# Kernel tuning notes

Hardware: AMD Instinct MI355X
Metric: run time of the kernel (lower is better)

The kernel has to match this reference:

```python
import jax, jax.numpy as jnp
import numpy as np

N = 50000          # nodes (num_sensors)
E = 600000         # edges
IN_DIM = 75        # 3 * 25
DIMS = [(75, 128), (128, 128), (128, 32)]  # (in, out) per layer: in->hidden->hidden->bottleneck


def setup_inputs() -> dict:
    key = jax.random.key(0)
    ks = jax.random.split(key, 4 + 5 * len(DIMS))
    inp = {
        "x": jax.random.normal(ks[0], (N, IN_DIM), dtype=jnp.float32),
        "edge_index": jax.random.randint(ks[1], (2, E), 0, N, dtype=jnp.int64),
        "weight": jax.random.uniform(ks[2], (E,), dtype=jnp.float32),
        "sim": jax.random.normal(ks[3], (E, 2), dtype=jnp.float32),
    }
    i = 4
    for l, (cin, cout) in enumerate(DIMS):
        s = jnp.float32(1.0 / np.sqrt(cin))
        inp[f"wr{l}"] = jax.random.normal(ks[i + 0], (cin, cout), dtype=jnp.float32) * s  # real part of complex conv filter
        inp[f"wi{l}"] = jax.random.normal(ks[i + 1], (cin, cout), dtype=jnp.float32) * s  # imag part
        inp[f"cb{l}"] = jnp.zeros((cout,), dtype=jnp.float32)                              # conv bias
        inp[f"lw{l}"] = jax.random.normal(ks[i + 2], (cout, cin), dtype=jnp.float32) * s  # Linear weight (torch layout [out,in])
        inp[f"lb{l}"] = jnp.zeros((cout,), dtype=jnp.float32)                              # Linear bias
        i += 5
    return inp


def _layer(x, src, dst, cr, ci, wr, wi, cb, lw, lb):
    # ModeConvFast: gather source features, scale by complex edge coefficient
    # c = weight * (sim_r + i*sim_i), scatter-add to destination nodes,
    # project with complex filter W = wr + i*wi, keep real part, add bias.
    xs = x[src]                                   # [E, Cin] gather
    agg_r = jax.ops.segment_sum(xs * cr[:, None], dst, num_segments=N)  # [N, Cin]
    agg_i = jax.ops.segment_sum(xs * ci[:, None], dst, num_segments=N)  # [N, Cin]
    conv = agg_r @ wr - agg_i @ wi + cb           # real part of complex matmul
    return jax.nn.relu(conv + x @ lw.T + lb)      # conv(x,...) + lin(x), then relu


def reference(x, edge_index, weight, sim,
              wr0, wi0, cb0, lw0, lb0,
              wr1, wi1, cb1, lw1, lb1,
              wr2, wi2, cb2, lw2, lb2):
    src, dst = edge_index[0], edge_index[1]
    cr = weight * sim[:, 0]                       # [E] real edge coefficient
    ci = weight * sim[:, 1]                       # [E] imag edge coefficient
    layers = [
        (wr0, wi0, cb0, lw0, lb0),
        (wr1, wi1, cb1, lw1, lb1),
        (wr2, wi2, cb2, lw2, lb2),
    ]
    for p in layers:
        x = _layer(x, src, dst, cr, ci, *p)
    return x
```

## Files before the change

kernel.cpp:

```cpp
#include <hip/hip_runtime.h>

#define N_NODES 50000
#define N_EDGES 600000
#define E_PAD_MAX (N_EDGES + N_NODES * 7)

using bf16x8 = __attribute__((ext_vector_type(8))) short;
using f32x4  = __attribute__((ext_vector_type(4))) float;
typedef unsigned int uint32_tt;

__device__ __forceinline__ unsigned short f2bf(float f) {
    union { float f; unsigned int u; } v; v.f = f;
    unsigned int u = v.u;
    return (unsigned short)((u + 0x7fffu + ((u >> 16) & 1u)) >> 16);
}
__device__ __forceinline__ float bf2f(unsigned int h16) {
    union { unsigned int u; float f; } v; v.u = h16 << 16;
    return v.f;
}


__global__ void hist_kernel(const int* __restrict__ ei, int* __restrict__ cnt, int E) {
    int e = blockIdx.x * 256 + threadIdx.x;
    if (e < E) atomicAdd(&cnt[ei[E + e]], 1);
}

__global__ void scan1(const int* __restrict__ deg, int* __restrict__ out,
                      int* __restrict__ bsum, int n) {
    __shared__ int s[256];
    int t = threadIdx.x;
    int base = blockIdx.x * 1024 + t * 4;
    int v0 = (base + 0 < n) ? ((deg[base + 0] + 7) & ~7) : 0;
    int v1 = (base + 1 < n) ? ((deg[base + 1] + 7) & ~7) : 0;
    int v2 = (base + 2 < n) ? ((deg[base + 2] + 7) & ~7) : 0;
    int v3 = (base + 3 < n) ? ((deg[base + 3] + 7) & ~7) : 0;
    int tsum = v0 + v1 + v2 + v3;
    s[t] = tsum;
    __syncthreads();
    for (int off = 1; off < 256; off <<= 1) {
        int tmp = (t >= off) ? s[t - off] : 0;
        __syncthreads();
        s[t] += tmp;
        __syncthreads();
    }
    int excl = s[t] - tsum;
    if (base + 0 < n) out[base + 0] = excl;
    if (base + 1 < n) out[base + 1] = excl + v0;
    if (base + 2 < n) out[base + 2] = excl + v0 + v1;
    if (base + 3 < n) out[base + 3] = excl + v0 + v1 + v2;
    if (t == 255) bsum[blockIdx.x] = s[255];
}

__global__ void scan2(int* __restrict__ bsum, int nb) {
    if (threadIdx.x == 0 && blockIdx.x == 0) {
        int acc = 0;
        for (int i = 0; i < nb; ++i) { int v = bsum[i]; bsum[i] = acc; acc += v; }
        bsum[nb] = acc;
    }
}

__global__ void scan3(int* __restrict__ off, const int* __restrict__ bsum, int n, int nb) {
    int i = blockIdx.x * 256 + threadIdx.x;
    if (i < n) off[i] += bsum[i >> 10];
    if (i == n) off[n] = bsum[nb];
}

__global__ void scatter_kernel(const int* __restrict__ ei, const float* __restrict__ w,
                               const float* __restrict__ sim, const int* __restrict__ off,
                               int* __restrict__ cnt, uint2* __restrict__ edat, int E) {
    int e = blockIdx.x * 256 + threadIdx.x;
    if (e >= E) return;
    int s = ei[e], d = ei[E + e];
    int p = off[d] + atomicAdd(&cnt[d], 1);
    float wt = w[e];
    uint2 m;
    m.x = (unsigned)s;
    m.y = (uint32_tt)f2bf(wt * sim[2 * e]) |
          ((uint32_tt)f2bf(wt * sim[2 * e + 1]) << 16);
    edat[p] = m;
}


__global__ void convert_x(const float* __restrict__ x0, unsigned short* __restrict__ xb, int n) {
    int i = blockIdx.x * 256 + threadIdx.x;
    if (i >= n * 96) return;
    int r = i / 96, c = i - r * 96;
    xb[i] = (c < 75) ? f2bf(x0[r * 75 + c]) : (unsigned short)0;
}

__global__ void build_bt(const float* __restrict__ wr, const float* __restrict__ wi,
                         const float* __restrict__ lw, unsigned short* __restrict__ BT,
                         int CIN, int CINP, int COUT) {
    int KTOT = 3 * CINP;
    int i = blockIdx.x * 256 + threadIdx.x;
    if (i >= COUT * KTOT) return;
    int nn = i / KTOT, k = i - nn * KTOT;
    int part = k / CINP, kk = k - part * CINP;
    float v = 0.f;
    if (kk < CIN) {
        if (part == 0)      v = wr[kk * COUT + nn];
        else if (part == 1) v = -wi[kk * COUT + nn];
        else                v = lw[nn * CIN + kk];
    }
    BT[i] = f2bf(v);
}

__global__ void build_bty(const float* __restrict__ wr, const float* __restrict__ wi,
                          const float* __restrict__ lw, unsigned short* __restrict__ BT) {
    int i = blockIdx.x * 256 + threadIdx.x;
    if (i >= 96 * 128) return;
    int nn = i >> 7, k = i & 127;
    float v;
    if (nn < 32)      v = wr[k * 32 + nn];
    else if (nn < 64) v = -wi[k * 32 + (nn - 32)];
    else              v = lw[(nn - 64) * 128 + k];
    BT[i] = f2bf(v);
}

template <int CU2>
__global__ __launch_bounds__(256) void agg_bf16(
    const uint32_tt* __restrict__ x, const int* __restrict__ off,
    const uint2* __restrict__ edat, uint32_tt* __restrict__ aggR,
    uint32_tt* __restrict__ aggI, int n) {
    int wave = threadIdx.x >> 6;
    int lane = threadIdx.x & 63;
    int node = __builtin_amdgcn_readfirstlane(blockIdx.x * 4 + wave);
    if (node >= n) return;
    int lc = (CU2 == 64) ? lane : (lane < CU2 ? lane : CU2 - 1);
    float arl = 0.f, arh = 0.f, ail = 0.f, aih = 0.f;
    int e0 = __builtin_amdgcn_readfirstlane(off[node]);
    int e1 = __builtin_amdgcn_readfirstlane(off[node + 1]);

    if (e0 < e1) {
        uint2 m[8];
#pragma unroll
        for (int j = 0; j < 8; ++j) m[j] = edat[e0 + j];
        for (int e = e0; e < e1; e += 8) {
            int sj[8]; float crj[8], cij[8];
#pragma unroll
            for (int j = 0; j < 8; ++j) {
                sj[j] = __builtin_amdgcn_readfirstlane((int)m[j].x);
                int pk = __builtin_amdgcn_readfirstlane((int)m[j].y);
                crj[j] = bf2f((unsigned)pk & 0xffffu);
                cij[j] = bf2f((unsigned)pk >> 16);
            }
            uint32_tt w[8];
#pragma unroll
            for (int j = 0; j < 8; ++j) {
                const uint32_tt* rowp = x + (size_t)sj[j] * CU2;
                w[j] = rowp[lc];
            }
            if (e + 8 < e1) {
#pragma unroll
                for (int j = 0; j < 8; ++j) m[j] = edat[e + 8 + j];
            }
#pragma unroll
            for (int j = 0; j < 8; ++j) {
                float lo = bf2f(w[j] & 0xffffu), hi = bf2f(w[j] >> 16);
                arl += crj[j] * lo; arh += crj[j] * hi;
                ail += cij[j] * lo; aih += cij[j] * hi;
            }
        }
    }
    if (lane < CU2) {
        aggR[(size_t)node * CU2 + lane] = (uint32_tt)f2bf(arl) | ((uint32_tt)f2bf(arh) << 16);
        aggI[(size_t)node * CU2 + lane] = (uint32_tt)f2bf(ail) | ((uint32_tt)f2bf(aih) << 16);
    }
}

__global__ __launch_bounds__(256) void agg_out(
    const uint32_tt* __restrict__ Y, const int* __restrict__ off,
    const uint2* __restrict__ edat, const float* __restrict__ cb,
    const float* __restrict__ lb, float* __restrict__ out, int n) {
    int wave = threadIdx.x >> 6;
    int lane = threadIdx.x & 63;
    int node = __builtin_amdgcn_readfirstlane(blockIdx.x * 4 + wave);
    if (node >= n) return;
    int lc = (lane < 32) ? lane : 31;
    int usei = (lane >> 4) & 1;
    float alo = 0.f, ahi = 0.f;
    int e0 = __builtin_amdgcn_readfirstlane(off[node]);
    int e1 = __builtin_amdgcn_readfirstlane(off[node + 1]);

    if (e0 < e1) {
        uint2 m[8];
#pragma unroll
        for (int j = 0; j < 8; ++j) m[j] = edat[e0 + j];
        for (int e = e0; e < e1; e += 8) {
            int sj[8]; float crj[8], cij[8];
#pragma unroll
            for (int j = 0; j < 8; ++j) {
                sj[j] = __builtin_amdgcn_readfirstlane((int)m[j].x);
                int pk = __builtin_amdgcn_readfirstlane((int)m[j].y);
                crj[j] = bf2f((unsigned)pk & 0xffffu);
                cij[j] = bf2f((unsigned)pk >> 16);
            }
            uint32_tt w[8];
#pragma unroll
            for (int j = 0; j < 8; ++j) {
                const uint32_tt* rowp = Y + (size_t)sj[j] * 48;
                w[j] = rowp[lc];
            }
            if (e + 8 < e1) {
#pragma unroll
                for (int j = 0; j < 8; ++j) m[j] = edat[e + 8 + j];
            }
#pragma unroll
            for (int j = 0; j < 8; ++j) {
                float c = usei ? cij[j] : crj[j];
                float lo = bf2f(w[j] & 0xffffu), hi = bf2f(w[j] >> 16);
                alo += c * lo; ahi += c * hi;
            }
        }
    }
    alo += __shfl_xor(alo, 16);
    ahi += __shfl_xor(ahi, 16);
    if (lane < 16) {
        uint32_tt lin = Y[(size_t)node * 48 + 32 + lane];
        int c0 = 2 * lane, c1 = 2 * lane + 1;
        float v0 = alo + bf2f(lin & 0xffffu) + cb[c0] + lb[c0];
        float v1 = ahi + bf2f(lin >> 16) + cb[c1] + lb[c1];
        float2 r;
        r.x = v0 > 0.f ? v0 : 0.f;
        r.y = v1 > 0.f ? v1 : 0.f;
        ((float2*)out)[(size_t)node * 16 + lane] = r;
    }
}

template <int CINP, int COUT, int BM, int WM, int WN, int MT, int NT,
          bool OUT_BF16, bool RAW, int PARTS>
__global__ __launch_bounds__(256) void gemm_mfma(
    const unsigned short* __restrict__ A0, const unsigned short* __restrict__ A1,
    const unsigned short* __restrict__ A2, const unsigned short* __restrict__ BT,
    const float* __restrict__ cb, const float* __restrict__ lb,
    void* __restrict__ outv, int n) {
    constexpr int PK = 40;
    constexpr int KTOT = PARTS * CINP;
    constexpr int NCH = KTOT / 32;
    constexpr int CPP = CINP / 32;
    __shared__ unsigned short sA[BM][PK];
    __shared__ unsigned short sB[COUT][PK];

    int t = threadIdx.x;
    int lane = t & 63, wave = t >> 6;
    int wm = wave / WN, wn = wave % WN;
    int ml = lane & 15, kh = lane >> 4;
    int node0 = blockIdx.x * BM;

    const unsigned short* Asrc[3] = {A0, A1, A2};

    f32x4 acc[MT][NT];
#pragma unroll
    for (int mt = 0; mt < MT; ++mt)
#pragma unroll
        for (int nt = 0; nt < NT; ++nt) acc[mt][nt] = (f32x4){0.f, 0.f, 0.f, 0.f};

    for (int c = 0; c < NCH; ++c) {
        int part = (PARTS == 1) ? 0 : (c / CPP);
        int kk = (c - part * CPP) * 32;
        const unsigned short* __restrict__ Ap = Asrc[part];
        __syncthreads();
#pragma unroll
        for (int i = t; i < BM * 4; i += 256) {
            int r = i >> 2, q = i & 3;
            int node = node0 + r;
            if (node >= n) node = n - 1;
            *(uint4*)&sA[r][q * 8] =
                *(const uint4*)(Ap + (size_t)node * CINP + kk + q * 8);
        }
#pragma unroll
        for (int i = t; i < COUT * 4; i += 256) {
            int r = i >> 2, q = i & 3;
            *(uint4*)&sB[r][q * 8] =
                *(const uint4*)(BT + (size_t)r * KTOT + c * 32 + q * 8);
        }
        __syncthreads();
        bf16x8 af[MT], bfr[NT];
#pragma unroll
        for (int mt = 0; mt < MT; ++mt)
            af[mt] = *(const bf16x8*)&sA[wm * (MT * 16) + mt * 16 + ml][kh * 8];
#pragma unroll
        for (int nt = 0; nt < NT; ++nt)
            bfr[nt] = *(const bf16x8*)&sB[wn * (NT * 16) + nt * 16 + ml][kh * 8];
#pragma unroll
        for (int mt = 0; mt < MT; ++mt)
#pragma unroll
            for (int nt = 0; nt < NT; ++nt)
                acc[mt][nt] = __builtin_amdgcn_mfma_f32_16x16x32_bf16(
                    af[mt], bfr[nt], acc[mt][nt], 0, 0, 0);
    }

    int row0 = kh * 4;
#pragma unroll
    for (int nt = 0; nt < NT; ++nt) {
        int col = wn * (NT * 16) + nt * 16 + ml;
        float bias = RAW ? 0.f : (cb[col] + lb[col]);
#pragma unroll
        for (int mt = 0; mt < MT; ++mt) {
#pragma unroll
            for (int r = 0; r < 4; ++r) {
                int node = node0 + wm * (MT * 16) + mt * 16 + row0 + r;
                if (node < n) {
                    float v = acc[mt][nt][r] + bias;
                    if (!RAW) v = v > 0.f ? v : 0.f;
                    if (OUT_BF16)
                        ((unsigned short*)outv)[(size_t)node * COUT + col] = f2bf(v);
                    else
                        ((float*)outv)[(size_t)node * COUT + col] = v;
                }
            }
        }
    }
}


extern "C" void kernel_launch(void* const* d_in, const int* in_sizes, int n_in,
                              void* d_out, int out_size, void* d_ws, size_t ws_size,
                              hipStream_t stream) {
    const float* x0  = (const float*)d_in[0];
    const int*   ei  = (const int*)d_in[1];
    const float* wgt = (const float*)d_in[2];
    const float* sim = (const float*)d_in[3];
    const float *wr[3], *wi[3], *cb[3], *lw[3], *lb[3];
    for (int l = 0; l < 3; ++l) {
        wr[l] = (const float*)d_in[4 + 5 * l];
        wi[l] = (const float*)d_in[5 + 5 * l];
        cb[l] = (const float*)d_in[6 + 5 * l];
        lw[l] = (const float*)d_in[7 + 5 * l];
        lb[l] = (const float*)d_in[8 + 5 * l];
    }

    char* p = (char*)d_ws;
    auto alloc = [&](size_t bytes) -> void* {
        void* r = p;
        p += (bytes + 255) & ~(size_t)255;
        return r;
    };
    int*   off  = (int*)alloc((N_NODES + 1) * 4);
    int*   cnt  = (int*)alloc(N_NODES * 4);
    int*   bsum = (int*)alloc(256);
    uint2* edat = (uint2*)alloc((size_t)E_PAD_MAX * 8);
    unsigned short* xb    = (unsigned short*)alloc((size_t)N_NODES * 96 * 2);
    unsigned short* aggRb = (unsigned short*)alloc((size_t)N_NODES * 128 * 2);
    unsigned short* aggIb = (unsigned short*)alloc((size_t)N_NODES * 128 * 2);
    unsigned short* h1b   = (unsigned short*)alloc((size_t)N_NODES * 128 * 2);
    unsigned short* h2b   = (unsigned short*)alloc((size_t)N_NODES * 128 * 2);
    unsigned short* Yb    = (unsigned short*)alloc((size_t)N_NODES * 96 * 2);
    unsigned short* BT0   = (unsigned short*)alloc((size_t)128 * 288 * 2);
    unsigned short* BT1   = (unsigned short*)alloc((size_t)128 * 384 * 2);
    unsigned short* BT2   = (unsigned short*)alloc((size_t)96 * 128 * 2);
    float* outp = (float*)d_out;

    hipMemsetAsync(cnt, 0, N_NODES * 4, stream);
    hipMemsetAsync(edat, 0, (size_t)E_PAD_MAX * 8, stream);
    hist_kernel<<<(N_EDGES + 255) / 256, 256, 0, stream>>>(ei, cnt, N_EDGES);
    int nb = (N_NODES + 1023) / 1024;
    scan1<<<nb, 256, 0, stream>>>(cnt, off, bsum, N_NODES);
    scan2<<<1, 64, 0, stream>>>(bsum, nb);
    scan3<<<(N_NODES + 1 + 255) / 256, 256, 0, stream>>>(off, bsum, N_NODES, nb);
    hipMemsetAsync(cnt, 0, N_NODES * 4, stream);
    scatter_kernel<<<(N_EDGES + 255) / 256, 256, 0, stream>>>(ei, wgt, sim, off, cnt,
                                                              edat, N_EDGES);
    convert_x<<<(N_NODES * 96 + 255) / 256, 256, 0, stream>>>(x0, xb, N_NODES);
    build_bt<<<(128 * 288 + 255) / 256, 256, 0, stream>>>(wr[0], wi[0], lw[0], BT0, 75, 96, 128);
    build_bt<<<(128 * 384 + 255) / 256, 256, 0, stream>>>(wr[1], wi[1], lw[1], BT1, 128, 128, 128);
    build_bty<<<(96 * 128 + 255) / 256, 256, 0, stream>>>(wr[2], wi[2], lw[2], BT2);

    int agrid = (N_NODES + 3) / 4;

    agg_bf16<48><<<agrid, 256, 0, stream>>>((const uint32_tt*)xb, off, edat,
                                            (uint32_tt*)aggRb, (uint32_tt*)aggIb, N_NODES);
    gemm_mfma<96, 128, 64, 2, 2, 2, 4, true, false, 3>
        <<<(N_NODES + 63) / 64, 256, 0, stream>>>(aggRb, aggIb, xb, BT0, cb[0], lb[0],
                                                  h1b, N_NODES);
    agg_bf16<64><<<agrid, 256, 0, stream>>>((const uint32_tt*)h1b, off, edat,
                                            (uint32_tt*)aggRb, (uint32_tt*)aggIb, N_NODES);
    gemm_mfma<128, 128, 64, 2, 2, 2, 4, true, false, 3>
        <<<(N_NODES + 63) / 64, 256, 0, stream>>>(aggRb, aggIb, h1b, BT1, cb[1], lb[1],
                                                  h2b, N_NODES);
    gemm_mfma<128, 96, 64, 2, 2, 2, 3, true, true, 1>
        <<<(N_NODES + 63) / 64, 256, 0, stream>>>(h2b, h2b, h2b, BT2, cb[2], lb[2],
                                                  Yb, N_NODES);
    agg_out<<<agrid, 256, 0, stream>>>((const uint32_tt*)Yb, off, edat, cb[2], lb[2],
                                       outp, N_NODES);
}
```

Before: 297.7 us.

## Fuse prep kernels, fold cnt reset into scan, and enlarge GEMM row tiles

Merges the x conversion and the three weight-packing kernels into one prep kernel, and zeroes the count array inside scan3 so a separate memset is no longer needed. This removes several launches and their gaps. It also doubles the GEMM row tile from 64 to 128 rows per block, with more M-fragments per warp, which halves the grid. The larger tile raises register pressure and leaves fewer blocks to spread across CUs.

```diff
diff --git a/kernel.cpp b/kernel.cpp
--- a/kernel.cpp
+++ b/kernel.cpp
@@ -58,9 +58,10 @@
     }
 }
 
-__global__ void scan3(int* __restrict__ off, const int* __restrict__ bsum, int n, int nb) {
+__global__ void scan3(int* __restrict__ off, const int* __restrict__ bsum,
+                      int* __restrict__ cnt, int n, int nb) {
     int i = blockIdx.x * 256 + threadIdx.x;
-    if (i < n) off[i] += bsum[i >> 10];
+    if (i < n) { off[i] += bsum[i >> 10]; cnt[i] = 0; }
     if (i == n) off[n] = bsum[nb];
 }
 
@@ -79,41 +80,54 @@
     edat[p] = m;
 }
 
-
-__global__ void convert_x(const float* __restrict__ x0, unsigned short* __restrict__ xb, int n) {
+__global__ void prep_kernel(
+    const float* __restrict__ x0, unsigned short* __restrict__ xb,
+    const float* __restrict__ wr0, const float* __restrict__ wi0,
+    const float* __restrict__ lw0, unsigned short* __restrict__ BT0,
+    const float* __restrict__ wr1, const float* __restrict__ wi1,
+    const float* __restrict__ lw1, unsigned short* __restrict__ BT1,
+    const float* __restrict__ wr2, const float* __restrict__ wi2,
+    const float* __restrict__ lw2, unsigned short* __restrict__ BT2, int n) {
     int i = blockIdx.x * 256 + threadIdx.x;
-    if (i >= n * 96) return;
-    int r = i / 96, c = i - r * 96;
-    xb[i] = (c < 75) ? f2bf(x0[r * 75 + c]) : (unsigned short)0;
-}
-
-__global__ void build_bt(const float* __restrict__ wr, const float* __restrict__ wi,
-                         const float* __restrict__ lw, unsigned short* __restrict__ BT,
-                         int CIN, int CINP, int COUT) {
-    int KTOT = 3 * CINP;
-    int i = blockIdx.x * 256 + threadIdx.x;
-    if (i >= COUT * KTOT) return;
-    int nn = i / KTOT, k = i - nn * KTOT;
-    int part = k / CINP, kk = k - part * CINP;
-    float v = 0.f;
-    if (kk < CIN) {
-        if (part == 0)      v = wr[kk * COUT + nn];
-        else if (part == 1) v = -wi[kk * COUT + nn];
-        else                v = lw[nn * CIN + kk];
-    }
-    BT[i] = f2bf(v);
-}
-
-__global__ void build_bty(const float* __restrict__ wr, const float* __restrict__ wi,
-                          const float* __restrict__ lw, unsigned short* __restrict__ BT) {
-    int i = blockIdx.x * 256 + threadIdx.x;
-    if (i >= 96 * 128) return;
-    int nn = i >> 7, k = i & 127;
-    float v;
-    if (nn < 32)      v = wr[k * 32 + nn];
-    else if (nn < 64) v = -wi[k * 32 + (nn - 32)];
-    else              v = lw[(nn - 64) * 128 + k];
-    BT[i] = f2bf(v);
+    int nconv = n * 96;
+    if (i < nconv) {
+        int r = i / 96, c = i - r * 96;
+        xb[i] = (c < 75) ? f2bf(x0[r * 75 + c]) : (unsigned short)0;
+        return;
+    }
+    i -= nconv;
+    if (i < 128 * 288) {
+        int nn = i / 288, k = i - nn * 288;
+        int part = k / 96, kk = k - part * 96;
+        float v = 0.f;
+        if (kk < 75) {
+            if (part == 0)      v = wr0[kk * 128 + nn];
+            else if (part == 1) v = -wi0[kk * 128 + nn];
+            else                v = lw0[nn * 75 + kk];
+        }
+        BT0[i] = f2bf(v);
+        return;
+    }
+    i -= 128 * 288;
+    if (i < 128 * 384) {
+        int nn = i / 384, k = i - nn * 384;
+        int part = k >> 7, kk = k & 127;
+        float v;
+        if (part == 0)      v = wr1[kk * 128 + nn];
+        else if (part == 1) v = -wi1[kk * 128 + nn];
+        else                v = lw1[nn * 128 + kk];
+        BT1[i] = f2bf(v);
+        return;
+    }
+    i -= 128 * 384;
+    if (i < 96 * 128) {
+        int nn = i >> 7, k = i & 127;
+        float v;
+        if (nn < 32)      v = wr2[k * 32 + nn];
+        else if (nn < 64) v = -wi2[k * 32 + (nn - 32)];
+        else              v = lw2[(nn - 64) * 128 + k];
+        BT2[i] = f2bf(v);
+    }
 }
 
 template <int CU2>
@@ -356,30 +370,31 @@
     int nb = (N_NODES + 1023) / 1024;
     scan1<<<nb, 256, 0, stream>>>(cnt, off, bsum, N_NODES);
     scan2<<<1, 64, 0, stream>>>(bsum, nb);
-    scan3<<<(N_NODES + 1 + 255) / 256, 256, 0, stream>>>(off, bsum, N_NODES, nb);
-    hipMemsetAsync(cnt, 0, N_NODES * 4, stream);
+    scan3<<<(N_NODES + 1 + 255) / 256, 256, 0, stream>>>(off, bsum, cnt, N_NODES, nb);
     scatter_kernel<<<(N_EDGES + 255) / 256, 256, 0, stream>>>(ei, wgt, sim, off, cnt,
                                                               edat, N_EDGES);
-    convert_x<<<(N_NODES * 96 + 255) / 256, 256, 0, stream>>>(x0, xb, N_NODES);
-    build_bt<<<(128 * 288 + 255) / 256, 256, 0, stream>>>(wr[0], wi[0], lw[0], BT0, 75, 96, 128);
-    build_bt<<<(128 * 384 + 255) / 256, 256, 0, stream>>>(wr[1], wi[1], lw[1], BT1, 128, 128, 128);
-    build_bty<<<(96 * 128 + 255) / 256, 256, 0, stream>>>(wr[2], wi[2], lw[2], BT2);
+    {
+        int total = N_NODES * 96 + 128 * 288 + 128 * 384 + 96 * 128;
+        prep_kernel<<<(total + 255) / 256, 256, 0, stream>>>(
+            x0, xb, wr[0], wi[0], lw[0], BT0, wr[1], wi[1], lw[1], BT1,
+            wr[2], wi[2], lw[2], BT2, N_NODES);
+    }
 
     int agrid = (N_NODES + 3) / 4;
 
     agg_bf16<48><<<agrid, 256, 0, stream>>>((const uint32_tt*)xb, off, edat,
                                             (uint32_tt*)aggRb, (uint32_tt*)aggIb, N_NODES);
-    gemm_mfma<96, 128, 64, 2, 2, 2, 4, true, false, 3>
-        <<<(N_NODES + 63) / 64, 256, 0, stream>>>(aggRb, aggIb, xb, BT0, cb[0], lb[0],
-                                                  h1b, N_NODES);
+    gemm_mfma<96, 128, 128, 2, 2, 4, 4, true, false, 3>
+        <<<(N_NODES + 127) / 128, 256, 0, stream>>>(aggRb, aggIb, xb, BT0, cb[0], lb[0],
+                                                    h1b, N_NODES);
     agg_bf16<64><<<agrid, 256, 0, stream>>>((const uint32_tt*)h1b, off, edat,
                                             (uint32_tt*)aggRb, (uint32_tt*)aggIb, N_NODES);
-    gemm_mfma<128, 128, 64, 2, 2, 2, 4, true, false, 3>
-        <<<(N_NODES + 63) / 64, 256, 0, stream>>>(aggRb, aggIb, h1b, BT1, cb[1], lb[1],
-                                                  h2b, N_NODES);
-    gemm_mfma<128, 96, 64, 2, 2, 2, 3, true, true, 1>
-        <<<(N_NODES + 63) / 64, 256, 0, stream>>>(h2b, h2b, h2b, BT2, cb[2], lb[2],
-                                                  Yb, N_NODES);
+    gemm_mfma<128, 128, 128, 2, 2, 4, 4, true, false, 3>
+        <<<(N_NODES + 127) / 128, 256, 0, stream>>>(aggRb, aggIb, h1b, BT1, cb[1], lb[1],
+                                                    h2b, N_NODES);
+    gemm_mfma<128, 96, 128, 2, 2, 4, 3, true, true, 1>
+        <<<(N_NODES + 127) / 128, 256, 0, stream>>>(h2b, h2b, h2b, BT2, cb[2], lb[2],
+                                                    Yb, N_NODES);
     agg_out<<<agrid, 256, 0, stream>>>((const uint32_tt*)Yb, off, edat, cb[2], lb[2],
                                        outp, N_NODES);
 }
```

After: 294.9 us. About the same (-0.9%).
